# Kernel tuning notes

Measured on AMD Instinct MI355X. Metric: run time of the kernel, lower is better.

The kernel has to match this reference:

```python
import jax, jax.numpy as jnp
import numpy as np

B, T, D_MODEL = 2, 2048, 1024
H, D = 16, 64
NEG = -1e9


def setup_inputs() -> dict:
    key = jax.random.key(0)
    k1, k2, k3 = jax.random.split(key, 3)
    x = jax.random.normal(k1, (B, T, D_MODEL), dtype=jnp.float32)
    # causal additive bias: 0 at valid (j<=i), large negative otherwise
    causal = jnp.tril(jnp.ones((T, T), dtype=bool))
    mask = jnp.where(causal, 0.0, NEG).astype(jnp.float32)[None, None]
    # params (torch Linear no-bias; stored as [in, out] so y = x @ W)
    W_qkv = jax.random.normal(k2, (D_MODEL, H * 5 * D), dtype=jnp.float32) / np.sqrt(D_MODEL)
    W_out = jax.random.normal(k3, (H * D, D_MODEL), dtype=jnp.float32) / np.sqrt(H * D)
    lam = jnp.full((H,), 0.8, dtype=jnp.float32)
    return {"x": x, "mask": mask, "W_qkv": W_qkv, "W_out": W_out, "lam": lam}


def reference(x, mask, W_qkv, W_out, lam):
    scale = np.sqrt(D).astype(np.float32)
    qkv = (x @ W_qkv).reshape(B, T, H, 5 * D)          # (B,T,H,5D)
    q1, q2, k1, k2, v = (qkv[..., i * D:(i + 1) * D] for i in range(5))
    # scores: (B,H,T,T)
    s1 = jnp.einsum('bihd,bjhd->bhij', q1, k1) / scale + mask
    s2 = jnp.einsum('bihd,bjhd->bhij', q2, k2) / scale + mask
    a1 = jax.nn.softmax(s1, axis=-1)
    a2 = jax.nn.softmax(s2, axis=-1)
    lam_c = jnp.clip(lam, 0.0, 1.0)[None, :, None, None]
    attn = a1 - lam_c * a2
    out = jnp.einsum('bhij,bjhd->bihd', attn, v).reshape(B, T, H * D)
    return out @ W_out
```

## Files before the change

kernel.cpp:

```cpp
#include <hip/hip_runtime.h>


typedef __attribute__((ext_vector_type(8))) short short8;
typedef __attribute__((ext_vector_type(4))) short short4v;
typedef __attribute__((ext_vector_type(4))) float floatx4;
typedef __attribute__((ext_vector_type(2))) unsigned uintx2;

#define MFMA16(A_, B_, C_) __builtin_amdgcn_mfma_f32_16x16x32_bf16((A_), (B_), (C_), 0, 0, 0)

#if __has_builtin(__builtin_amdgcn_mfma_f32_16x16x16_bf16)
#define PVMFMA(A_, B_, C_) __builtin_amdgcn_mfma_f32_16x16x16_bf16((A_), (B_), (C_), 0, 0, 0)
#elif __has_builtin(__builtin_amdgcn_mfma_f32_16x16x16bf16_1k)
#define PVMFMA(A_, B_, C_) __builtin_amdgcn_mfma_f32_16x16x16bf16_1k((A_), (B_), (C_), 0, 0, 0)
#else
__device__ __forceinline__ floatx4 pvmfma_asm(short4v a, short4v b, floatx4 c) {
  asm("v_mfma_f32_16x16x16_bf16 %0, %1, %2, %0\n\ts_nop 7" : "+v"(c) : "v"(a), "v"(b));
  return c;
}
#define PVMFMA(A_, B_, C_) pvmfma_asm((A_), (B_), (C_))
#endif

__device__ __forceinline__ unsigned short f2bf(float f) {
  unsigned u;
  __builtin_memcpy(&u, &f, 4);
  u += 0x7fffu + ((u >> 16) & 1u);
  return (unsigned short)(u >> 16);
}

__device__ __forceinline__ unsigned packbf2(float a, float b) {
  unsigned ua, ub;
  __builtin_memcpy(&ua, &a, 4);
  __builtin_memcpy(&ub, &b, 4);
  ua += 0x8000u;
  ub += 0x8000u;
  return __builtin_amdgcn_perm(ub, ua, 0x07060302u);
}

__device__ __forceinline__ void gload16(const unsigned short* g, void* l) {
  __builtin_amdgcn_global_load_lds(
      (const __attribute__((address_space(1))) void*)g,
      (__attribute__((address_space(3))) void*)l, 16, 0, 0);
}

__global__ __launch_bounds__(256) void cast_f32_bf16(const float* __restrict__ in,
                                                     unsigned short* __restrict__ out) {
  size_t i = ((size_t)blockIdx.x * 256 + threadIdx.x) * 8;
  float4 a0 = *(const float4*)(in + i);
  float4 a1 = *(const float4*)(in + i + 4);
  short8 v = {(short)f2bf(a0.x), (short)f2bf(a0.y), (short)f2bf(a0.z), (short)f2bf(a0.w),
              (short)f2bf(a1.x), (short)f2bf(a1.y), (short)f2bf(a1.z), (short)f2bf(a1.w)};
  *(short8*)(out + i) = v;
}

__global__ __launch_bounds__(256) void transpose_both(const float* __restrict__ wqkv,
                                                      unsigned short* __restrict__ wqkvT,
                                                      const float* __restrict__ wout,
                                                      unsigned short* __restrict__ woutT) {
  __shared__ unsigned short t[32][33];
  int bid = blockIdx.x;
  const float* in;
  unsigned short* out;
  int R = 1024, C;
  int bx, by;
  if (bid < 5120) {
    in = wqkv; out = wqkvT; C = 5120;
    bx = bid % 160; by = bid / 160;
  } else {
    bid -= 5120;
    in = wout; out = woutT; C = 1024;
    bx = bid % 32; by = bid / 32;
  }
  int c0 = bx * 32, r0 = by * 32;
  int tx = threadIdx.x & 31, ty = threadIdx.x >> 5;
#pragma unroll
  for (int i = 0; i < 4; i++) {
    int r = ty + i * 8;
    t[r][tx] = f2bf(in[(size_t)(r0 + r) * C + c0 + tx]);
  }
  __syncthreads();
#pragma unroll
  for (int i = 0; i < 4; i++) {
    int r = ty + i * 8;
    out[(size_t)(c0 + r) * R + r0 + tx] = t[tx][r];
  }
}

__global__ __launch_bounds__(512, 2) void gemm_qkv(const unsigned short* __restrict__ A,
                                                   const unsigned short* __restrict__ Bt,
                                                   unsigned short* __restrict__ qkbuf,
                                                   unsigned short* __restrict__ vtbuf) {
  const int tid = threadIdx.x;
  const int wave = tid >> 6, lane = tid & 63, lane15 = lane & 15, quad = lane >> 4;
  const int wm = wave >> 2, wn = wave & 3;
  const int bn = blockIdx.x % 20, bm = blockIdx.x / 20;
  const int row0 = bm * 256, col0 = bn * 256;
  __shared__ __align__(16) short SMEM[65536];
  floatx4 acc[8][4] = {};

  const int srow = lane >> 3;
  const int sseg = ((lane & 7) ^ srow) * 8;
  const unsigned short* gA = A + (size_t)(row0 + srow) * 1024 + sseg;
  const unsigned short* gB = Bt + (size_t)(col0 + srow) * 1024 + sseg;

  auto stage = [&](int bufidx, int kt) {
#pragma unroll
    for (int u = 0; u < 4; u++) {
      const int c = wave * 4 + u;
      gload16(gA + (size_t)c * 8192 + kt, &SMEM[bufidx * 16384 + c * 512]);
      gload16(gB + (size_t)c * 8192 + kt, &SMEM[32768 + bufidx * 16384 + c * 512]);
    }
  };

  stage(0, 0);
  stage(1, 64);

  const int swz = (lane15 & 7) << 3;
  for (int t = 0; t < 16; t++) {
    if (t < 15) {
      asm volatile("s_waitcnt vmcnt(8)" ::: "memory");
    } else {
      asm volatile("s_waitcnt vmcnt(0)" ::: "memory");
    }
    __builtin_amdgcn_s_barrier();
    const short* Ab = &SMEM[(t & 1) * 16384];
    const short* Bb = &SMEM[32768 + (t & 1) * 16384];
#pragma unroll
    for (int kh = 0; kh < 2; kh++) {
      short8 bf[4];
#pragma unroll
      for (int nt = 0; nt < 4; nt++)
        bf[nt] =
            *(const short8*)&Bb[(wn * 64 + nt * 16 + lane15) * 64 + ((kh * 32 + quad * 8) ^ swz)];
#pragma unroll
      for (int mh = 0; mh < 2; mh++) {
        short8 af[4];
#pragma unroll
        for (int mt = 0; mt < 4; mt++)
          af[mt] = *(const short8*)&Ab[(wm * 128 + mh * 64 + mt * 16 + lane15) * 64 +
                                       ((kh * 32 + quad * 8) ^ swz)];
        __builtin_amdgcn_s_setprio(1);
#pragma unroll
        for (int mt = 0; mt < 4; mt++)
#pragma unroll
          for (int nt = 0; nt < 4; nt++)
            acc[mh * 4 + mt][nt] = MFMA16(af[mt], bf[nt], acc[mh * 4 + mt][nt]);
        __builtin_amdgcn_s_setprio(0);
      }
    }
    __builtin_amdgcn_s_barrier();
    if (t + 2 < 16) stage(t & 1, (t + 2) * 64);
  }

  const int G = bn * 4 + wn;
  const int g5 = G % 5, h = G / 5;
  short* Svt = SMEM;
  if (g5 != 4) {
#pragma unroll
    for (int m = 0; m < 8; m++)
#pragma unroll
      for (int nt = 0; nt < 4; nt++)
#pragma unroll
        for (int r = 0; r < 4; r++) {
          const int row = row0 + wm * 128 + m * 16 + quad * 4 + r;
          const int cq = g5 * 64 + nt * 16 + lane15;
          qkbuf[(size_t)row * 4096 + h * 256 + cq] = f2bf(acc[m][nt][r]);
        }
  } else {
#pragma unroll
    for (int m = 0; m < 8; m++)
#pragma unroll
      for (int nt = 0; nt < 4; nt++)
#pragma unroll
        for (int r = 0; r < 4; r++)
          Svt[(nt * 16 + lane15) * 264 + wm * 128 + m * 16 + quad * 4 + r] =
              (short)f2bf(acc[m][nt][r]);
  }
  __syncthreads();
  if ((bn % 5) != 0) {
    const int wnV = (4 + bn) % 5;
    const int hV = (4 * bn + wnV) / 5;
    const int bb = row0 >> 11, t0 = row0 & 2047;
    const int d = tid >> 3, sg = (tid & 7) * 32;
    unsigned short* gdst = vtbuf + (size_t)((bb * 16 + hV) * 64 + d) * 2048 + t0 + sg;
#pragma unroll
    for (int u2 = 0; u2 < 4; u2++)
      *(short8*)(gdst + u2 * 8) = *(const short8*)&Svt[d * 264 + sg + u2 * 8];
  }
}

__global__ __launch_bounds__(512, 4) void attn_kernel(const unsigned short* __restrict__ qk,
                                                      const unsigned short* __restrict__ vt,
                                                      const float* __restrict__ lam,
                                                      unsigned short* __restrict__ attnout) {
  const int tid = threadIdx.x;
  const int wave = tid >> 6, lane = tid & 63, lane15 = lane & 15, quad = lane >> 4;
  const int w4 = wave & 3, wt = wave >> 2;
  const int bid = blockIdx.x;
  const int u = bid >> 8, c = bid & 255, k = c >> 5, bh = c & 31;
  const int pr = u ? (15 - k) : k;
  const int h = bh & 15, b = bh >> 4;
  const int qt = wt ? (31 - pr) : pr;

  __shared__ __align__(16) short K12s[2][64 * 128];
  __shared__ __align__(16) short Vts[2][64 * 64];
  __shared__ __align__(16) short Ls[8][16 * 68];

  const float lamv = fminf(fmaxf(lam[h], 0.0f), 1.0f);

  const unsigned short* kbase = qk + (size_t)(b * 2048) * 4096 + h * 256 + 128;
  const unsigned short* vbase = vt + (size_t)((b * 16 + h) * 64) * 2048;

  const int klr = lane >> 4, kcp = (lane & 15) * 16;
  const int vlr = lane >> 3, vcp = (lane & 7) * 16;
  const int swz = (lane15 & 7) << 4;

  const int qrow0 = qt * 64 + w4 * 16;
  const unsigned short* qb = qk + (size_t)(b * 2048 + qrow0 + lane15) * 4096 + h * 256;
  const short8 q1f0 = *(const short8*)(qb + quad * 8);
  const short8 q1f1 = *(const short8*)(qb + 32 + quad * 8);
  const short8 q2f0 = *(const short8*)(qb + 64 + quad * 8);
  const short8 q2f1 = *(const short8*)(qb + 96 + quad * 8);

  floatx4 o1[4] = {}, o2[4] = {};
  float lp1 = 0.f, lp2 = 0.f;

  const int qsub = qt * 4 + w4;
  const int njt = 32 - pr;

#pragma unroll
  for (int u2 = 0; u2 < 2; u2++) {
    const int ck = wave * 2 + u2, row = 4 * ck + klr;
    gload16(kbase + (size_t)row * 4096 + ((kcp ^ ((row & 7) << 4)) >> 1), &K12s[0][ck * 512]);
  }
  {
    const int cv = wave, row = 8 * cv + vlr;
    gload16(vbase + (size_t)row * 2048 + ((vcp ^ ((row & 7) << 4)) >> 1), &Vts[0][cv * 512]);
  }

  int cur = 0;
  for (int jt = 0; jt < njt; jt++) {
    __syncthreads();
    if (jt + 1 < njt) {
      const int nb = cur ^ 1;
#pragma unroll
      for (int u2 = 0; u2 < 2; u2++) {
        const int ck = wave * 2 + u2, row = 4 * ck + klr;
        gload16(kbase + (size_t)((jt + 1) * 64 + row) * 4096 + ((kcp ^ ((row & 7) << 4)) >> 1),
                &K12s[nb][ck * 512]);
      }
      {
        const int cv = wave, row = 8 * cv + vlr;
        gload16(vbase + (size_t)row * 2048 + (jt + 1) * 64 + ((vcp ^ ((row & 7) << 4)) >> 1),
                &Vts[nb][cv * 512]);
      }
    }

    const int rel = qsub - 4 * jt;
    if (rel >= 0) {
#pragma unroll
      for (int mat = 0; mat < 2; mat++) {
        const int koffB = mat ? 128 : 0;
        const short8 qf0 = mat ? q2f0 : q1f0;
        const short8 qf1 = mat ? q2f1 : q1f1;
        float* lp = mat ? &lp2 : &lp1;
        floatx4* oo = mat ? o2 : o1;

#pragma unroll
        for (int ms = 0; ms < 4; ms++) {
          if (ms <= rel) {
            const short* kr = &K12s[cur][(ms * 16 + lane15) * 128];
            short8 k0 = *(const short8*)(kr + (((koffB + quad * 16) ^ swz) >> 1));
            short8 k1 = *(const short8*)(kr + (((koffB + 64 + quad * 16) ^ swz) >> 1));
            floatx4 s = {0.f, 0.f, 0.f, 0.f};
            s = MFMA16(k0, qf0, s);
            s = MFMA16(k1, qf1, s);
            float e[4];
#pragma unroll
            for (int r = 0; r < 4; r++)
              e[r] = __builtin_amdgcn_exp2f(s[r] * 0.18033688011112042f);
            if (ms == rel) {
              const int jq = quad * 4;
#pragma unroll
              for (int r = 0; r < 4; r++) e[r] = (jq + r <= lane15) ? e[r] : 0.0f;
            }
            *lp += (e[0] + e[1]) + (e[2] + e[3]);
            uintx2 wv = {packbf2(e[0], e[1]), packbf2(e[2], e[3])};
            short4v bv;
            __builtin_memcpy(&bv, &wv, 8);
            const int vcol = ((ms * 32 + quad * 8) ^ swz) >> 1;
#pragma unroll
            for (int nt = 0; nt < 4; nt++) {
              const short4v av = *(const short4v*)&Vts[cur][(nt * 16 + lane15) * 64 + vcol];
              oo[nt] = PVMFMA(av, bv, oo[nt]);
            }
          }
        }
      }
    }
    cur ^= 1;
  }

  lp1 += __shfl_xor(lp1, 16, 64);
  lp1 += __shfl_xor(lp1, 32, 64);
  lp2 += __shfl_xor(lp2, 16, 64);
  lp2 += __shfl_xor(lp2, 32, 64);

  const float rl1 = __builtin_amdgcn_rcpf(lp1);
  const float rl2 = lamv * __builtin_amdgcn_rcpf(lp2);
  short* L = &Ls[wave][0];
#pragma unroll
  for (int nt = 0; nt < 4; nt++) {
    float v0 = o1[nt][0] * rl1 - o2[nt][0] * rl2;
    float v1 = o1[nt][1] * rl1 - o2[nt][1] * rl2;
    float v2 = o1[nt][2] * rl1 - o2[nt][2] * rl2;
    float v3 = o1[nt][3] * rl1 - o2[nt][3] * rl2;
    uintx2 wv = {packbf2(v0, v1), packbf2(v2, v3)};
    *(uintx2*)&L[lane15 * 68 + nt * 16 + quad * 4] = wv;
  }
#pragma unroll
  for (int r2 = 0; r2 < 4; r2++) {
    const uintx2 ov = *(const uintx2*)&L[(quad * 4 + r2) * 68 + lane15 * 4];
    const int row = b * 2048 + qrow0 + quad * 4 + r2;
    *(uintx2*)&attnout[(size_t)row * 1024 + h * 64 + lane15 * 4] = ov;
  }
}

__global__ __launch_bounds__(256) void gemm_out(const unsigned short* __restrict__ A,
                                                const unsigned short* __restrict__ Bt,
                                                float* __restrict__ Cout) {
  const int tid = threadIdx.x;
  const int wave = tid >> 6, lane = tid & 63, lane15 = lane & 15, quad = lane >> 4;
  const int wr = wave >> 1, wc = wave & 1;
  const int bn = blockIdx.x & 7, bm = blockIdx.x >> 3;
  const int row0 = bm * 64, col0 = bn * 128;
  __shared__ __align__(16) short As[64 * 64];
  __shared__ __align__(16) short Bs[128 * 64];
  floatx4 acc[2][4] = {};
  const int slr = lane >> 3, scl = (lane & 7) * 8;
  for (int kt = 0; kt < 1024; kt += 64) {
    __syncthreads();
#pragma unroll
    for (int u = 0; u < 2; u++) {
      const int c = wave * 2 + u;
      gload16(A + (size_t)(row0 + 8 * c + slr) * 1024 + kt + scl, &As[c * 512]);
    }
#pragma unroll
    for (int u = 0; u < 4; u++) {
      const int c = wave * 4 + u;
      gload16(Bt + (size_t)(col0 + 8 * c + slr) * 1024 + kt + scl, &Bs[c * 512]);
    }
    __syncthreads();
#pragma unroll
    for (int kh = 0; kh < 2; kh++) {
      short8 af[2], bf[4];
#pragma unroll
      for (int mt = 0; mt < 2; mt++)
        af[mt] = *(const short8*)&As[(wr * 32 + mt * 16 + lane15) * 64 + kh * 32 + quad * 8];
#pragma unroll
      for (int nt = 0; nt < 4; nt++)
        bf[nt] = *(const short8*)&Bs[(wc * 64 + nt * 16 + lane15) * 64 + kh * 32 + quad * 8];
#pragma unroll
      for (int mt = 0; mt < 2; mt++)
#pragma unroll
        for (int nt = 0; nt < 4; nt++) acc[mt][nt] = MFMA16(af[mt], bf[nt], acc[mt][nt]);
    }
  }
#pragma unroll
  for (int mt = 0; mt < 2; mt++)
#pragma unroll
    for (int nt = 0; nt < 4; nt++)
#pragma unroll
      for (int r = 0; r < 4; r++) {
        int row = row0 + wr * 32 + mt * 16 + quad * 4 + r;
        int col = col0 + wc * 64 + nt * 16 + lane15;
        Cout[(size_t)row * 1024 + col] = acc[mt][nt][r];
      }
}

extern "C" void kernel_launch(void* const* d_in, const int* in_sizes, int n_in,
                              void* d_out, int out_size, void* d_ws, size_t ws_size,
                              hipStream_t stream) {
  const float* x = (const float*)d_in[0];
  const float* Wqkv = (const float*)d_in[2];
  const float* Wout = (const float*)d_in[3];
  const float* lam = (const float*)d_in[4];
  float* out = (float*)d_out;

  unsigned short* ws = (unsigned short*)d_ws;
  unsigned short* WqkvT = ws;
  unsigned short* WoutT = WqkvT + (size_t)5120 * 1024;
  unsigned short* qkbuf = WoutT + (size_t)1024 * 1024;
  unsigned short* vtbuf = qkbuf + (size_t)4096 * 4096;
  unsigned short* xb = vtbuf + (size_t)2 * 16 * 64 * 2048;
  unsigned short* attnbuf = xb;

  cast_f32_bf16<<<2048, 256, 0, stream>>>(x, xb);
  transpose_both<<<5120 + 1024, 256, 0, stream>>>(Wqkv, WqkvT, Wout, WoutT);
  gemm_qkv<<<16 * 20, 512, 0, stream>>>(xb, WqkvT, qkbuf, vtbuf);
  attn_kernel<<<512, 512, 0, stream>>>(qkbuf, vtbuf, lam, attnbuf);
  gemm_out<<<64 * 8, 256, 0, stream>>>(attnbuf, WoutT, out);
}
```

Before: 245.7 us.

## Prefetch K/V two tiles ahead with explicit vmcnt waits; merge prep kernels

Merges the x cast kernel and the weight transpose kernel into a single prep launch, saving one kernel launch. In the attention loop, K/V tiles are now staged two iterations ahead. The implicit __syncthreads is replaced by explicit s_waitcnt vmcnt(3)/lgkmcnt(0) and raw s_barrier calls, so global loads for a later tile can stay in flight during compute. This relies on the hand-counted vmcnt matching the three gload16 issued per stage, which is fragile if the compiler emits other vector memory ops.

```diff
diff --git a/kernel.cpp b/kernel.cpp
--- a/kernel.cpp
+++ b/kernel.cpp
@@ -42,22 +42,24 @@
       (__attribute__((address_space(3))) void*)l, 16, 0, 0);
 }
 
-__global__ __launch_bounds__(256) void cast_f32_bf16(const float* __restrict__ in,
-                                                     unsigned short* __restrict__ out) {
-  size_t i = ((size_t)blockIdx.x * 256 + threadIdx.x) * 8;
-  float4 a0 = *(const float4*)(in + i);
-  float4 a1 = *(const float4*)(in + i + 4);
-  short8 v = {(short)f2bf(a0.x), (short)f2bf(a0.y), (short)f2bf(a0.z), (short)f2bf(a0.w),
-              (short)f2bf(a1.x), (short)f2bf(a1.y), (short)f2bf(a1.z), (short)f2bf(a1.w)};
-  *(short8*)(out + i) = v;
-}
-
-__global__ __launch_bounds__(256) void transpose_both(const float* __restrict__ wqkv,
-                                                      unsigned short* __restrict__ wqkvT,
-                                                      const float* __restrict__ wout,
-                                                      unsigned short* __restrict__ woutT) {
+__global__ __launch_bounds__(256) void prep(const float* __restrict__ x,
+                                            unsigned short* __restrict__ xb,
+                                            const float* __restrict__ wqkv,
+                                            unsigned short* __restrict__ wqkvT,
+                                            const float* __restrict__ wout,
+                                            unsigned short* __restrict__ woutT) {
+  int bid = blockIdx.x;
+  if (bid < 2048) {
+    size_t i = ((size_t)bid * 256 + threadIdx.x) * 8;
+    float4 a0 = *(const float4*)(x + i);
+    float4 a1 = *(const float4*)(x + i + 4);
+    short8 v = {(short)f2bf(a0.x), (short)f2bf(a0.y), (short)f2bf(a0.z), (short)f2bf(a0.w),
+                (short)f2bf(a1.x), (short)f2bf(a1.y), (short)f2bf(a1.z), (short)f2bf(a1.w)};
+    *(short8*)(xb + i) = v;
+    return;
+  }
+  bid -= 2048;
   __shared__ unsigned short t[32][33];
-  int bid = blockIdx.x;
   const float* in;
   unsigned short* out;
   int R = 1024, C;
@@ -214,6 +216,20 @@
   const int vlr = lane >> 3, vcp = (lane & 7) * 16;
   const int swz = (lane15 & 7) << 4;
 
+  auto stageKV = [&](int buf, int jt) {
+#pragma unroll
+    for (int u2 = 0; u2 < 2; u2++) {
+      const int ck = wave * 2 + u2, row = 4 * ck + klr;
+      gload16(kbase + (size_t)(jt * 64 + row) * 4096 + ((kcp ^ ((row & 7) << 4)) >> 1),
+              &K12s[buf][ck * 512]);
+    }
+    {
+      const int cv = wave, row = 8 * cv + vlr;
+      gload16(vbase + (size_t)row * 2048 + jt * 64 + ((vcp ^ ((row & 7) << 4)) >> 1),
+              &Vts[buf][cv * 512]);
+    }
+  };
+
   const int qrow0 = qt * 64 + w4 * 16;
   const unsigned short* qb = qk + (size_t)(b * 2048 + qrow0 + lane15) * 4096 + h * 256;
   const short8 q1f0 = *(const short8*)(qb + quad * 8);
@@ -227,34 +243,18 @@
   const int qsub = qt * 4 + w4;
   const int njt = 32 - pr;
 
-#pragma unroll
-  for (int u2 = 0; u2 < 2; u2++) {
-    const int ck = wave * 2 + u2, row = 4 * ck + klr;
-    gload16(kbase + (size_t)row * 4096 + ((kcp ^ ((row & 7) << 4)) >> 1), &K12s[0][ck * 512]);
-  }
-  {
-    const int cv = wave, row = 8 * cv + vlr;
-    gload16(vbase + (size_t)row * 2048 + ((vcp ^ ((row & 7) << 4)) >> 1), &Vts[0][cv * 512]);
-  }
-
-  int cur = 0;
+  stageKV(0, 0);
+  stageKV(1, 1);
+
   for (int jt = 0; jt < njt; jt++) {
-    __syncthreads();
     if (jt + 1 < njt) {
-      const int nb = cur ^ 1;
-#pragma unroll
-      for (int u2 = 0; u2 < 2; u2++) {
-        const int ck = wave * 2 + u2, row = 4 * ck + klr;
-        gload16(kbase + (size_t)((jt + 1) * 64 + row) * 4096 + ((kcp ^ ((row & 7) << 4)) >> 1),
-                &K12s[nb][ck * 512]);
-      }
-      {
-        const int cv = wave, row = 8 * cv + vlr;
-        gload16(vbase + (size_t)row * 2048 + (jt + 1) * 64 + ((vcp ^ ((row & 7) << 4)) >> 1),
-                &Vts[nb][cv * 512]);
-      }
-    }
-
+      asm volatile("s_waitcnt vmcnt(3)" ::: "memory");
+    } else {
+      asm volatile("s_waitcnt vmcnt(0)" ::: "memory");
+    }
+    __builtin_amdgcn_s_barrier();
+
+    const int cur = jt & 1;
     const int rel = qsub - 4 * jt;
     if (rel >= 0) {
 #pragma unroll
@@ -297,7 +297,9 @@
         }
       }
     }
-    cur ^= 1;
+    asm volatile("s_waitcnt lgkmcnt(0)" ::: "memory");
+    __builtin_amdgcn_s_barrier();
+    if (jt + 2 < njt) stageKV(cur, jt + 2);
   }
 
   lp1 += __shfl_xor(lp1, 16, 64);
@@ -394,8 +396,7 @@
   unsigned short* xb = vtbuf + (size_t)2 * 16 * 64 * 2048;
   unsigned short* attnbuf = xb;
 
-  cast_f32_bf16<<<2048, 256, 0, stream>>>(x, xb);
-  transpose_both<<<5120 + 1024, 256, 0, stream>>>(Wqkv, WqkvT, Wout, WoutT);
+  prep<<<2048 + 6144, 256, 0, stream>>>(x, xb, Wqkv, WqkvT, Wout, WoutT);
   gemm_qkv<<<16 * 20, 512, 0, stream>>>(xb, WqkvT, qkbuf, vtbuf);
   attn_kernel<<<512, 512, 0, stream>>>(qkbuf, vtbuf, lam, attnbuf);
   gemm_out<<<64 * 8, 256, 0, stream>>>(attnbuf, WoutT, out);
```

After: 247.0 us. About the same (+0.5%).
